# Performance work log

Hardware: AMD Instinct MI355X
Metric: run time of the kernel (lower is better)

Reference implementation:

```python
import jax, jax.numpy as jnp
import numpy as np
from jax import lax


def _median_blur(img, k):
    # img: [B, H, W]; k odd (3 here). Replicate border like cv2.medianBlur.
    p = k // 2
    B, H, W = img.shape
    xp = jnp.pad(img, ((0, 0), (p, p), (p, p)), mode='edge')
    # Gather the k*k shifted views -> [B, H, W, k*k]
    wins = jnp.stack([xp[:, i:i + H, j:j + W] for i in range(k) for j in range(k)], axis=-1)
    return jnp.median(wins, axis=-1)


def setup_inputs() -> dict:
    key = jax.random.key(0)
    kx, kt = jax.random.split(key)
    x = jax.random.normal(kx, (32, 1, 512, 512), dtype=jnp.float32)
    t_tensor = jax.random.randint(kt, (32,), 0, 10).astype(jnp.int64)
    return {"x": x, "t_tensor": t_tensor, "kernel_size": 3, "num_timesteps": 10}


def reference(x, t_tensor, kernel_size, num_timesteps):
    # Faithful vectorized version of MedianBlur.forward_process:
    # sample i gets t_tensor[i] successive median blurs.
    B, C, H, W = x.shape  # C == 1, matching the .squeeze() in the original
    img = x[:, 0, :, :]  # [B, H, W]
    t = t_tensor.astype(jnp.int32)

    def step(cur, j):
        blurred = _median_blur(cur, kernel_size)
        active = (j < t)[:, None, None]  # only samples with t_i > j keep blurring
        return jnp.where(active, blurred, cur), None

    out, _ = lax.scan(step, img, jnp.arange(num_timesteps, dtype=jnp.int32))
    return out[:, None, :, :]  # restore channel dim, like unsqueeze(0) per sample
```

## Files before the change

### kernel.cpp

```cpp
#include <hip/hip_runtime.h>


#define TD 58
#define OW 40
#define P  7
#define RAD 9
#define NT 64

__device__ __forceinline__ float min3f(float a, float b, float c) { return fminf(fminf(a, b), c); }
__device__ __forceinline__ float max3f(float a, float b, float c) { return fmaxf(fmaxf(a, b), c); }
__device__ __forceinline__ float med3f(float a, float b, float c) { return __builtin_amdgcn_fmed3f(a, b, c); }

__global__ __launch_bounds__(NT, 3) void median_fused_kernel(
    const float* __restrict__ src, float* __restrict__ dst,
    const int* __restrict__ t)
{
    __shared__ float buf[TD * TD];

    const int b   = blockIdx.y;
    const int ty  = blockIdx.x / 13;
    const int tx  = blockIdx.x - ty * 13;
    const int y0  = ty * OW;
    const int x0  = tx * OW;
    const int tid = threadIdx.x;
    const float* img  = src + (b << 18);
    float*       outb = dst + (b << 18);

    int T = t[b];
    T = min(max(T, 0), 9);

    if (T == 0) {
        for (int idx = tid; idx < 400; idx += NT) {
            int row = idx / 10, c4 = idx - row * 10;
            int gy = y0 + row, gx = x0 + (c4 << 2);
            if (gy < 512 && gx < 512)
                *(float4*)&outb[(gy << 9) + gx] =
                    *(const float4*)&img[(gy << 9) + gx];
        }
        return;
    }

    for (int i = tid; i < TD * TD; i += NT) {
        int r = i / TD, c = i - r * TD;
        int gy = min(max(y0 - RAD + r, 0), 511);
        int gx = min(max(x0 - RAD + c, 0), 511);
        buf[i] = img[(gy << 9) + gx];
    }

    const int ptx = tid & 7;
    const int pty = tid >> 3;
    const int ub  = 1 + P * pty;
    const int vb  = 1 + P * ptx;

    const bool padTop = (y0 == 0)   && (pty == 1);
    const bool padBot = (y0 == 480) && (pty == 5);
    const bool padLft = (x0 == 0)   && (ptx == 1);
    const bool padRgt = (x0 == 480) && (ptx == 5);

    __syncthreads();

    float stage[49];
    #pragma unroll
    for (int i = 0; i < 7; ++i)
        #pragma unroll
        for (int j = 0; j < 7; ++j)
            stage[i * 7 + j] = buf[(ub + i) * TD + vb + j];

    for (int k = 0; k < T; ++k) {
        float A[9], Br[9], C[9];
        {
            const float* p = &buf[(ub - 1) * TD + (vb - 1)];
            #pragma unroll
            for (int j = 0; j < 9; ++j) A[j] = p[j];
        }
        Br[0] = buf[ub * TD + (vb - 1)];
        #pragma unroll
        for (int j = 0; j < 7; ++j) Br[1 + j] = stage[j];
        Br[8] = buf[ub * TD + (vb + 7)];

        #pragma unroll
        for (int i = 0; i < 7; ++i) {
            if (i < 6) {
                C[0] = buf[(ub + 1 + i) * TD + (vb - 1)];
                #pragma unroll
                for (int j = 0; j < 7; ++j) C[1 + j] = stage[(i + 1) * 7 + j];
                C[8] = buf[(ub + 1 + i) * TD + (vb + 7)];
            } else {
                const float* p = &buf[(ub + 7) * TD + (vb - 1)];
                #pragma unroll
                for (int j = 0; j < 9; ++j) C[j] = p[j];
            }
            float lo[9], mi[9], hi[9];
            #pragma unroll
            for (int j = 0; j < 9; ++j) {
                lo[j] = min3f(A[j], Br[j], C[j]);
                mi[j] = med3f(A[j], Br[j], C[j]);
                hi[j] = max3f(A[j], Br[j], C[j]);
            }
            #pragma unroll
            for (int j = 0; j < 7; ++j)
                stage[i * 7 + j] = med3f(max3f(lo[j], lo[j+1], lo[j+2]),
                                         med3f(mi[j], mi[j+1], mi[j+2]),
                                         min3f(hi[j], hi[j+1], hi[j+2]));
            #pragma unroll
            for (int j = 0; j < 9; ++j) { A[j] = Br[j]; Br[j] = C[j]; }
        }

        if (padTop) {
            #pragma unroll
            for (int j = 0; j < 7; ++j) stage[j] = stage[7 + j];
        }
        if (padBot) {
            #pragma unroll
            for (int j = 0; j < 7; ++j) stage[35 + j] = stage[28 + j];
        }
        if (padLft) {
            #pragma unroll
            for (int i = 0; i < 7; ++i) stage[i * 7 + 0] = stage[i * 7 + 1];
        }
        if (padRgt) {
            #pragma unroll
            for (int i = 0; i < 7; ++i) stage[i * 7 + 5] = stage[i * 7 + 4];
        }

        __syncthreads();

        if (k == T - 1) {
            #pragma unroll
            for (int i = 0; i < 7; ++i)
                #pragma unroll
                for (int j = 0; j < 7; ++j)
                    buf[(ub + i) * TD + vb + j] = stage[i * 7 + j];
        } else {
            #pragma unroll
            for (int j = 0; j < 7; ++j) {
                buf[ub * TD + vb + j]       = stage[j];
                buf[(ub + 6) * TD + vb + j] = stage[42 + j];
            }
            #pragma unroll
            for (int i = 1; i < 6; ++i) {
                buf[(ub + i) * TD + vb]     = stage[i * 7];
                buf[(ub + i) * TD + vb + 6] = stage[i * 7 + 6];
            }
        }

        __syncthreads();
    }

    for (int idx = tid; idx < 400; idx += NT) {
        int row = idx / 10, c4 = idx - row * 10;
        int gy = y0 + row, gx = x0 + (c4 << 2);
        if (gy < 512 && gx < 512) {
            const float* s = &buf[(RAD + row) * TD + RAD + (c4 << 2)];
            float4 v = { s[0], s[1], s[2], s[3] };
            *(float4*)&outb[(gy << 9) + gx] = v;
        }
    }
}

extern "C" void kernel_launch(void* const* d_in, const int* in_sizes, int n_in,
                              void* d_out, int out_size, void* d_ws, size_t ws_size,
                              hipStream_t stream) {
    const float* x   = (const float*)d_in[0];
    const int*   t   = (const int*)d_in[1];
    float*       out = (float*)d_out;

    dim3 block(NT);
    dim3 grid(169, 32);
    median_fused_kernel<<<grid, block, 0, stream>>>(x, out, t);
}
```

Baseline: 113.3 us.

## Use 4x4 per-thread patches with 256-thread blocks and in-compute border padding

Retiles the fused iterated median kernel: each block now uses 256 threads, each owning a 4x4 register patch instead of a 7x7 one, with a 48x48 output tile and a 66x66 shared halo. Image-border replication is folded into the window loads instead of being fixed up after each step. Interior values are written back to shared memory only once at the end. This cuts register pressure and raises occupancy and parallelism, at the cost of more halo traffic between threads and a larger shared-memory tile per block.

New measurement: 111.4 us. No clear change (-1.7%).

```diff
diff --git a/kernel.cpp b/kernel.cpp
--- a/kernel.cpp
+++ b/kernel.cpp
@@ -1,25 +1,24 @@
 #include <hip/hip_runtime.h>
 
 
-#define TD 58
-#define OW 40
-#define P  7
+#define TD  66
+#define OW  48
 #define RAD 9
-#define NT 64
+#define NT  256
 
-__device__ __forceinline__ float min3f(float a, float b, float c) { return fminf(fminf(a, b), c); }
-__device__ __forceinline__ float max3f(float a, float b, float c) { return fmaxf(fmaxf(a, b), c); }
-__device__ __forceinline__ float med3f(float a, float b, float c) { return __builtin_amdgcn_fmed3f(a, b, c); }
+static __device__ __forceinline__ float min3f(float a, float b, float c) { return fminf(fminf(a, b), c); }
+static __device__ __forceinline__ float max3f(float a, float b, float c) { return fmaxf(fmaxf(a, b), c); }
+static __device__ __forceinline__ float med3f(float a, float b, float c) { return __builtin_amdgcn_fmed3f(a, b, c); }
 
-__global__ __launch_bounds__(NT, 3) void median_fused_kernel(
+__global__ __launch_bounds__(NT, 8) void median_fused_kernel(
     const float* __restrict__ src, float* __restrict__ dst,
     const int* __restrict__ t)
 {
     __shared__ float buf[TD * TD];
 
     const int b   = blockIdx.y;
-    const int ty  = blockIdx.x / 13;
-    const int tx  = blockIdx.x - ty * 13;
+    const int ty  = blockIdx.x / 11;
+    const int tx  = blockIdx.x - ty * 11;
     const int y0  = ty * OW;
     const int x0  = tx * OW;
     const int tid = threadIdx.x;
@@ -30,8 +29,8 @@
     T = min(max(T, 0), 9);
 
     if (T == 0) {
-        for (int idx = tid; idx < 400; idx += NT) {
-            int row = idx / 10, c4 = idx - row * 10;
+        for (int idx = tid; idx < 576; idx += NT) {
+            int row = idx / 12, c4 = idx - row * 12;
             int gy = y0 + row, gx = x0 + (c4 << 2);
             if (gy < 512 && gx < 512)
                 *(float4*)&outb[(gy << 9) + gx] =
@@ -47,108 +46,107 @@
         buf[i] = img[(gy << 9) + gx];
     }
 
-    const int ptx = tid & 7;
-    const int pty = tid >> 3;
-    const int ub  = 1 + P * pty;
-    const int vb  = 1 + P * ptx;
+    const int ptx = tid & 15;
+    const int pty = tid >> 4;
+    const int ub  = 1 + (pty << 2);
+    const int vb  = 1 + (ptx << 2);
 
-    const bool padTop = (y0 == 0)   && (pty == 1);
-    const bool padBot = (y0 == 480) && (pty == 5);
-    const bool padLft = (x0 == 0)   && (ptx == 1);
-    const bool padRgt = (x0 == 480) && (ptx == 5);
+    const bool subTop = (y0 == 0)   && (pty == 2);
+    const bool subBot = (y0 == 480) && (pty == 9);
+    const bool subLft = (x0 == 0)   && (ptx == 2);
+    const bool subRgt = (x0 == 480) && (ptx == 9);
 
     __syncthreads();
 
-    float stage[49];
+    float stage[16];
     #pragma unroll
-    for (int i = 0; i < 7; ++i)
+    for (int i = 0; i < 4; ++i)
         #pragma unroll
-        for (int j = 0; j < 7; ++j)
-            stage[i * 7 + j] = buf[(ub + i) * TD + vb + j];
+        for (int j = 0; j < 4; ++j)
+            stage[i * 4 + j] = buf[(ub + i) * TD + vb + j];
 
     for (int k = 0; k < T; ++k) {
-        float A[9], Br[9], C[9];
+        float A[6], Br[6], C[6];
+
+        Br[1] = stage[0]; Br[2] = stage[1]; Br[3] = stage[2]; Br[4] = stage[3];
         {
+            const float* p = &buf[ub * TD + vb - 1];
+            Br[0] = subLft ? stage[0] : p[0];
+            Br[5] = subRgt ? stage[3] : p[5];
+        }
+        if (subTop) {
+            #pragma unroll
+            for (int j = 0; j < 6; ++j) A[j] = Br[j];
+        } else {
             const float* p = &buf[(ub - 1) * TD + (vb - 1)];
             #pragma unroll
-            for (int j = 0; j < 9; ++j) A[j] = p[j];
+            for (int j = 0; j < 6; ++j) A[j] = p[j];
+            if (subLft) A[0] = A[1];
+            if (subRgt) A[5] = A[4];
         }
-        Br[0] = buf[ub * TD + (vb - 1)];
-        #pragma unroll
-        for (int j = 0; j < 7; ++j) Br[1 + j] = stage[j];
-        Br[8] = buf[ub * TD + (vb + 7)];
 
         #pragma unroll
-        for (int i = 0; i < 7; ++i) {
-            if (i < 6) {
-                C[0] = buf[(ub + 1 + i) * TD + (vb - 1)];
+        for (int i = 0; i < 4; ++i) {
+            if (i < 3) {
+                const float* p = &buf[(ub + 1 + i) * TD + (vb - 1)];
+                C[1] = stage[(i + 1) * 4 + 0];
+                C[2] = stage[(i + 1) * 4 + 1];
+                C[3] = stage[(i + 1) * 4 + 2];
+                C[4] = stage[(i + 1) * 4 + 3];
+                C[0] = subLft ? C[1] : p[0];
+                C[5] = subRgt ? C[4] : p[5];
+            } else if (subBot) {
                 #pragma unroll
-                for (int j = 0; j < 7; ++j) C[1 + j] = stage[(i + 1) * 7 + j];
-                C[8] = buf[(ub + 1 + i) * TD + (vb + 7)];
+                for (int j = 0; j < 6; ++j) C[j] = Br[j];
             } else {
-                const float* p = &buf[(ub + 7) * TD + (vb - 1)];
+                const float* p = &buf[(ub + 4) * TD + (vb - 1)];
                 #pragma unroll
-                for (int j = 0; j < 9; ++j) C[j] = p[j];
+                for (int j = 0; j < 6; ++j) C[j] = p[j];
+                if (subLft) C[0] = C[1];
+                if (subRgt) C[5] = C[4];
             }
-            float lo[9], mi[9], hi[9];
+            float lo[6], mi[6], hi[6];
             #pragma unroll
-            for (int j = 0; j < 9; ++j) {
+            for (int j = 0; j < 6; ++j) {
                 lo[j] = min3f(A[j], Br[j], C[j]);
                 mi[j] = med3f(A[j], Br[j], C[j]);
                 hi[j] = max3f(A[j], Br[j], C[j]);
             }
             #pragma unroll
-            for (int j = 0; j < 7; ++j)
-                stage[i * 7 + j] = med3f(max3f(lo[j], lo[j+1], lo[j+2]),
+            for (int j = 0; j < 4; ++j)
+                stage[i * 4 + j] = med3f(max3f(lo[j], lo[j+1], lo[j+2]),
                                          med3f(mi[j], mi[j+1], mi[j+2]),
                                          min3f(hi[j], hi[j+1], hi[j+2]));
             #pragma unroll
-            for (int j = 0; j < 9; ++j) { A[j] = Br[j]; Br[j] = C[j]; }
-        }
-
-        if (padTop) {
-            #pragma unroll
-            for (int j = 0; j < 7; ++j) stage[j] = stage[7 + j];
-        }
-        if (padBot) {
-            #pragma unroll
-            for (int j = 0; j < 7; ++j) stage[35 + j] = stage[28 + j];
-        }
-        if (padLft) {
-            #pragma unroll
-            for (int i = 0; i < 7; ++i) stage[i * 7 + 0] = stage[i * 7 + 1];
-        }
-        if (padRgt) {
-            #pragma unroll
-            for (int i = 0; i < 7; ++i) stage[i * 7 + 5] = stage[i * 7 + 4];
+            for (int j = 0; j < 6; ++j) { A[j] = Br[j]; Br[j] = C[j]; }
         }
 
         __syncthreads();
 
-        if (k == T - 1) {
-            #pragma unroll
-            for (int i = 0; i < 7; ++i)
-                #pragma unroll
-                for (int j = 0; j < 7; ++j)
-                    buf[(ub + i) * TD + vb + j] = stage[i * 7 + j];
-        } else {
-            #pragma unroll
-            for (int j = 0; j < 7; ++j) {
-                buf[ub * TD + vb + j]       = stage[j];
-                buf[(ub + 6) * TD + vb + j] = stage[42 + j];
-            }
-            #pragma unroll
-            for (int i = 1; i < 6; ++i) {
-                buf[(ub + i) * TD + vb]     = stage[i * 7];
-                buf[(ub + i) * TD + vb + 6] = stage[i * 7 + 6];
-            }
-        }
+        buf[ub * TD + vb + 0]       = stage[0];
+        buf[ub * TD + vb + 1]       = stage[1];
+        buf[ub * TD + vb + 2]       = stage[2];
+        buf[ub * TD + vb + 3]       = stage[3];
+        buf[(ub + 3) * TD + vb + 0] = stage[12];
+        buf[(ub + 3) * TD + vb + 1] = stage[13];
+        buf[(ub + 3) * TD + vb + 2] = stage[14];
+        buf[(ub + 3) * TD + vb + 3] = stage[15];
+        buf[(ub + 1) * TD + vb + 0] = stage[4];
+        buf[(ub + 1) * TD + vb + 3] = stage[7];
+        buf[(ub + 2) * TD + vb + 0] = stage[8];
+        buf[(ub + 2) * TD + vb + 3] = stage[11];
 
         __syncthreads();
     }
 
-    for (int idx = tid; idx < 400; idx += NT) {
-        int row = idx / 10, c4 = idx - row * 10;
+    buf[(ub + 1) * TD + vb + 1] = stage[5];
+    buf[(ub + 1) * TD + vb + 2] = stage[6];
+    buf[(ub + 2) * TD + vb + 1] = stage[9];
+    buf[(ub + 2) * TD + vb + 2] = stage[10];
+    __syncthreads();
+
+    for (int idx = tid; idx < 576; idx += NT) {
+        int row = idx / 12, c4 = idx - row * 12;
         int gy = y0 + row, gx = x0 + (c4 << 2);
         if (gy < 512 && gx < 512) {
             const float* s = &buf[(RAD + row) * TD + RAD + (c4 << 2)];
@@ -166,6 +164,6 @@
     float*       out = (float*)d_out;
 
     dim3 block(NT);
-    dim3 grid(169, 32);
+    dim3 grid(121, 32);
     median_fused_kernel<<<grid, block, 0, stream>>>(x, out, t);
 }
```
